# Optimization experiments

Measured on AMD Instinct MI355X. Metric: run time of the kernel, lower is better.

## Reference

```python
import jax, jax.numpy as jnp
import numpy as np
from jax import lax

WIN_SIZE = 11
SIGMA = 1.5
WEIGHTS = jnp.array([0.0448, 0.2856, 0.3001, 0.2363, 0.1333], dtype=jnp.float32)
C1 = (0.01 * 1.0) ** 2  # val_range = 1.0
C2 = (0.03 * 1.0) ** 2


def gaussian_kernel2d(kernel_size, sigma):
    g = jnp.arange(kernel_size, dtype=jnp.float32) - kernel_size // 2
    g = jnp.exp(-(g ** 2) / (2.0 * sigma ** 2))
    g = g / g.sum()
    return jnp.outer(g, g)  # [k, k]


def depthwise_conv(x, k2d):
    # x: [B, C, H, W]; same gaussian window applied per-channel (groups=C), VALID padding
    C = x.shape[1]
    w = jnp.broadcast_to(k2d, (C, 1) + k2d.shape).astype(x.dtype)
    return lax.conv_general_dilated(x, w, (1, 1), 'VALID',
                                    feature_group_count=C,
                                    dimension_numbers=('NCHW', 'OIHW', 'NCHW'))


def ssim_index(x, y, k2d, nonnegative=True):
    # returns (ss, cs) each of shape [B, C] (spatial mean, per channel)
    m1 = depthwise_conv(x, k2d)
    m2 = depthwise_conv(y, k2d)
    m12 = m1 * m2
    m1s = m1 * m1
    m2s = m2 * m2
    v1 = depthwise_conv(x * x, k2d) - m1s
    v2 = depthwise_conv(y * y, k2d) - m2s
    cov = depthwise_conv(x * y, k2d) - m12
    cs = (2.0 * cov + C2) / (v1 + v2 + C2)
    ss = (2.0 * m12 + C1) / (m1s + m2s + C1) * cs
    ss = ss.reshape(ss.shape[0], ss.shape[1], -1).mean(axis=-1)
    cs = cs.reshape(cs.shape[0], cs.shape[1], -1).mean(axis=-1)
    if nonnegative:
        ss = jnp.maximum(ss, 0.0)
        cs = jnp.maximum(cs, 0.0)
    return ss, cs


def avg_pool2(x):
    # F.avg_pool2d(kernel_size=2). Input spatial dims are even at every scale
    # (512 -> 32), so ceil_mode never pads; plain 2x2/2 mean pooling is exact.
    s = lax.reduce_window(x, jnp.array(0.0, x.dtype), lax.add,
                          (1, 1, 2, 2), (1, 1, 2, 2), 'VALID')
    return s * 0.25


def setup_inputs() -> dict:
    key = jax.random.key(0)
    k1, k2 = jax.random.split(key)
    B, C, H, W = 4, 12, 512, 512
    pred = jax.random.normal(k1, (B, C, H, W), dtype=jnp.float32)
    target = jax.random.randint(k2, (B, H, W), 0, C, dtype=jnp.int64)
    return {"pred": pred, "target": target}


def reference(pred, target):
    # MS_SSIMLoss.forward with process_input=True, nonnegative=True.
    # The per-class python loop in the original is an independent depthwise
    # computation per channel -> vectorized here as a C-channel grouped conv;
    # loss = mean over classes of (1 - mean over batch of msss) == 1 - mean(msss).
    num_classes = pred.shape[1]
    x = jax.nn.softmax(pred, axis=1)
    y = jax.nn.one_hot(target, num_classes, dtype=pred.dtype).transpose(0, 3, 1, 2)
    k2d = gaussian_kernel2d(WIN_SIZE, SIGMA)
    m = WEIGHTS.shape[0]
    vals = []
    for i in range(m):
        if i > 0:
            x = avg_pool2(x)
            y = avg_pool2(y)
        ss, cs = ssim_index(x, y, k2d, nonnegative=True)
        vals.append(cs if i + 1 < m else ss)
    stacked = jnp.stack(vals, axis=-1)  # [B, C, m]
    msss = jnp.prod(stacked ** WEIGHTS, axis=-1)  # [B, C]
    return 1.0 - msss.mean()
```

## Files before the change

### kernel.cpp

```cpp
#include <hip/hip_runtime.h>

#define NCH 12
#define NB  4
#define BC  48
#define HW0 (512 * 512)

#define GK_INIT { 0.00102840f, 0.00759863f, 0.03600078f, 0.10936081f, \
                  0.21300541f, 0.26601164f, 0.21300541f, 0.10936081f, \
                  0.03600078f, 0.00759863f, 0.00102840f }

__global__ __launch_bounds__(256)
void k_prep(const float* __restrict__ pred, const int* __restrict__ tgt,
            float* __restrict__ U, float* __restrict__ X1,
            unsigned short* __restrict__ Y1, double* __restrict__ acc) {
    if (blockIdx.x == 0) {
        for (int t = threadIdx.x; t < 480; t += 256) acc[t] = 0.0;
    }
    const int blk = blockIdx.x;
    const int b  = blk >> 8;
    const int py = blk & 255;
    const int px = threadIdx.x;
    const size_t o00 = (size_t)(2 * py) * 512 + 2 * px;
    const size_t o10 = o00 + 512;
    const float* Pb = pred + (size_t)b * NCH * HW0;

    float ex[NCH], ey[NCH], ez[NCH], ew[NCH];
    float s00 = 0.f, s01 = 0.f, s10 = 0.f, s11 = 0.f;
#pragma unroll
    for (int c = 0; c < NCH; ++c) {
        const float* pc = Pb + (size_t)c * HW0;
        float2 r0 = *(const float2*)(pc + o00);
        float2 r1 = *(const float2*)(pc + o10);
        ex[c] = __expf(r0.x); ey[c] = __expf(r0.y);
        ez[c] = __expf(r1.x); ew[c] = __expf(r1.y);
        s00 += ex[c]; s01 += ey[c]; s10 += ez[c]; s11 += ew[c];
    }
    float u00 = 1.f / s00, u01 = 1.f / s01, u10 = 1.f / s10, u11 = 1.f / s11;
    float* Ub = U + (size_t)b * HW0;
    *(float2*)(Ub + o00) = make_float2(u00, u01);
    *(float2*)(Ub + o10) = make_float2(u10, u11);

    const int* Tb = tgt + (size_t)b * HW0;
    int2 t0 = *(const int2*)(Tb + o00);
    int2 t1 = *(const int2*)(Tb + o10);

#pragma unroll
    for (int c = 0; c < NCH; ++c) {
        float xs = ex[c] * u00 + ey[c] * u01 + ez[c] * u10 + ew[c] * u11;
        size_t oidx = ((size_t)(b * NCH + c) * 256 + py) * 256 + px;
        X1[oidx] = 0.25f * xs;
        unsigned cnt = (unsigned)(t0.x == c) + (unsigned)(t0.y == c)
                     + (unsigned)(t1.x == c) + (unsigned)(t1.y == c);
        Y1[oidx] = (unsigned short)(cnt << 6);
    }
}

union SMem {
    struct {
        float sx[42 * 43 + 4];
        uint2 tm4[42 * 35];
        unsigned long long ybits[30];
        float red[8];
    } s0;
    struct {
        unsigned int sxy[42 * 43 + 4];
        uint2 tm4[42 * 35];
        unsigned short tm5[42 * 35];
        float red[8];
    } rg;
};

__device__ __forceinline__ void ssim0_tile(
    const float* __restrict__ pred, const float* __restrict__ U,
    const int* __restrict__ tgt, double* __restrict__ acc,
    int tile, int bc,
    float* sx, uint2* tm4, unsigned long long* ybits, float* red) {
    constexpr int SS = 43;
    constexpr int TS = 35;
    constexpr int H = 512, W = 512, OH = 502, OW = 502, tilesX = 16;
    const float gk[11] = GK_INIT;

    const int ty = tile / tilesX, tx = tile - ty * tilesX;
    const int oy = ty * 32, ox = tx * 32;
    const int tid = threadIdx.x;
    const bool interior = (oy + 41 < H) && (ox + 41 < W);

    const int b = bc / NCH, cls = bc - (bc / NCH) * NCH;
    const float* Pb = pred + (((size_t)b * NCH + cls) << 18);
    const float* Ub = U + ((size_t)b << 18);
    const int* Tb = tgt + ((size_t)b << 18);

    {
        int r = tid / 42, c = tid - (tid / 42) * 42;
#pragma unroll
        for (int k = 0; k < 7; ++k) {
            bool inr = (k < 6) || (tid < 228);
            int gy = oy + r, gx = ox + c;
            bool ld = inr && (interior || (gy < H && gx < W));
            float xv = 0.f;
            bool bit = false;
            if (ld) {
                int off = gy * W + gx;
                xv = __expf(Pb[off]) * Ub[off];
                bit = (Tb[off] == cls);
            }
            unsigned long long mk = __ballot(bit);
            if ((tid & 63) == 0) ybits[(tid >> 6) + (k << 2)] = mk;
            if (inr) sx[r * SS + c] = xv;
            c += 4; r += 6;
            if (c >= 42) { c -= 42; r += 1; }
        }
        if (tid == 0) { ybits[28] = 0ull; ybits[29] = 0ull; }
    }
    __syncthreads();

    if (tid < 252) {
        int rr = tid / 6, s = tid - (tid / 6) * 6;
        int c0 = s * 6;
        const float* px = sx + rr * SS + c0;
        float ac0[6] = {}, ac1[6] = {}, ac2[6] = {}, ac3[6] = {};
        unsigned long long win;
        {
            int i0 = rr * 42 + c0;
            int w = i0 >> 6, sh = i0 & 63;
            unsigned long long lo = ybits[w], hi = ybits[w + 1];
            win = sh ? ((lo >> sh) | (hi << (64 - sh))) : lo;
        }
#pragma unroll
        for (int j = 0; j < 16; ++j) {
            float xv = px[j];
            float xx = xv * xv;
            bool bit = (win >> j) & 1;
            float yv = bit ? 1.f : 0.f;
            float xy = bit ? xv : 0.f;
#pragma unroll
            for (int o = 0; o < 6; ++o) {
                int kk = j - o;
                if (kk >= 0 && kk <= 10) {
                    float g = gk[kk];
                    ac0[o] = fmaf(g, xv, ac0[o]);
                    ac1[o] = fmaf(g, yv, ac1[o]);
                    ac2[o] = fmaf(g, xx, ac2[o]);
                    ac3[o] = fmaf(g, xy, ac3[o]);
                }
            }
        }
        int ob = rr * TS + c0;
#pragma unroll
        for (int o = 0; o < 6; ++o) {
            if (c0 + o < 32) {
                unsigned ua = __float_as_uint(ac0[o]);
                unsigned ub = __float_as_uint(ac1[o]);
                unsigned uc = __float_as_uint(ac2[o]);
                unsigned ud = __float_as_uint(ac3[o]);
                tm4[ob + o] = make_uint2((ua >> 16) | (ub & 0xFFFF0000u),
                                         (uc >> 16) | (ud & 0xFFFF0000u));
            }
        }
    }
    __syncthreads();

    const float C1 = 1e-4f, C2 = 9e-4f;
    const int cc = tid & 31, rg = tid >> 5, r0 = rg << 2;
    float a0[4] = {}, a1[4] = {}, a2[4] = {}, a3[4] = {};
    const int vb = r0 * TS + cc;
#pragma unroll
    for (int k = 0; k < 14; ++k) {
        uint2 tv = tm4[vb + k * TS];
        float m1v = __uint_as_float(tv.x << 16);
        float m2v = __uint_as_float(tv.x & 0xFFFF0000u);
        float xxv = __uint_as_float(tv.y << 16);
        float xyv = __uint_as_float(tv.y & 0xFFFF0000u);
#pragma unroll
        for (int j = 0; j < 4; ++j) {
            int kk = k - j;
            if (kk >= 0 && kk <= 10) {
                float g = gk[kk];
                a0[j] = fmaf(g, m1v, a0[j]);
                a1[j] = fmaf(g, m2v, a1[j]);
                a2[j] = fmaf(g, xxv, a2[j]);
                a3[j] = fmaf(g, xyv, a3[j]);
            }
        }
    }
    float cs_l = 0.f, ss_l = 0.f;
    const bool colok = (ox + cc < OW);
#pragma unroll
    for (int j = 0; j < 4; ++j) {
        if (colok && (oy + r0 + j < OH)) {
            float m1 = a0[j], m2 = a1[j];
            float sxx = a2[j], sxy_ = a3[j];
            float m11 = m1 * m1, m22 = m2 * m2, m12 = m1 * m2;
            float v1 = sxx - m11, v2 = m2 - m22, cov = sxy_ - m12;
            float d1 = m11 + m22 + C1, d2 = v1 + v2 + C2;
            float n2 = 2.f * cov + C2;
            float q = 1.f / (d1 * d2);
            cs_l = fmaf(n2 * d1, q, cs_l);
            ss_l = fmaf((2.f * m12 + C1) * n2, q, ss_l);
        }
    }

    for (int off = 32; off; off >>= 1) {
        cs_l += __shfl_down(cs_l, off);
        ss_l += __shfl_down(ss_l, off);
    }
    int wv = tid >> 6, ln = tid & 63;
    if (ln == 0) { red[wv] = cs_l; red[4 + wv] = ss_l; }
    __syncthreads();
    if (tid == 0) {
        double cs_b = (double)red[0] + (double)red[1] + (double)red[2] + (double)red[3];
        double ss_b = (double)red[4] + (double)red[5] + (double)red[6] + (double)red[7];
        atomicAdd(&acc[bc], cs_b);
        atomicAdd(&acc[48 + bc], ss_b);
    }
}

template <int PIN>
__device__ __forceinline__ void ssim_tile_g(
    const float* __restrict__ Xs, const unsigned short* __restrict__ Ys,
    int H, int W, int OH, int OW, int tilesX, int tile, int bc,
    double* __restrict__ acc, int scale,
    unsigned int* sxy, uint2* tm4, unsigned short* tm5, float* red) {
    constexpr int SS = 43;
    constexpr int TS = 35;
    const float gk[11] = GK_INIT;

    const int ty = tile / tilesX, tx = tile - ty * tilesX;
    const int oy = ty * 32, ox = tx * 32;
    const int tid = threadIdx.x;
    const bool interior = (oy + 41 < H) && (ox + 41 < W);

    constexpr int SC = 1 << PIN;
    const int SW = W * SC;
    const float* Xb = Xs + (size_t)bc * H * W * SC * SC;
    const unsigned short* Yb = Ys + (size_t)bc * H * W * SC * SC;

    {
        int r = tid / 42, c = tid - (tid / 42) * 42;
#pragma unroll
        for (int k = 0; k < 7; ++k) {
            bool inr = (k < 6) || (tid < 228);
            int gy = oy + r, gx = ox + c;
            bool ld = inr && (interior || (gy < H && gx < W));
            float xv = 0.f;
            unsigned yc = 0;
            if (ld) {
                if constexpr (PIN == 0) {
                    int off = gy * SW + gx;
                    xv = Xb[off];
                    yc = Yb[off];
                } else {
                    const float* q = Xb + (SC * gy) * SW + SC * gx;
                    const unsigned short* qy = Yb + (SC * gy) * SW + SC * gx;
                    float s = 0.f; unsigned us = 0;
#pragma unroll
                    for (int a = 0; a < SC; ++a) {
                        const float* qr = q + a * SW;
                        const unsigned short* qyr = qy + a * SW;
                        if constexpr (PIN == 1) {
                            float2 f = *(const float2*)qr;
                            s += f.x + f.y;
                            ushort2 uy = *(const ushort2*)qyr;
                            us += (unsigned)uy.x + (unsigned)uy.y;
                        } else {
#pragma unroll
                            for (int e4 = 0; e4 < SC / 4; ++e4) {
                                float4 f = *(const float4*)(qr + e4 * 4);
                                s += (f.x + f.y) + (f.z + f.w);
                                ushort4 uy = *(const ushort4*)(qyr + e4 * 4);
                                us += ((unsigned)uy.x + (unsigned)uy.y)
                                    + ((unsigned)uy.z + (unsigned)uy.w);
                            }
                        }
                    }
                    xv = s * (1.f / (float)(SC * SC));
                    yc = us >> (2 * PIN);
                }
            }
            if (inr) {
                unsigned xb = (__float_as_uint(xv) + 0x8000u) >> 16;
                sxy[r * SS + c] = (yc << 16) | xb;
            }
            c += 4; r += 6;
            if (c >= 42) { c -= 42; r += 1; }
        }
    }
    __syncthreads();

    if (tid < 252) {
        int rr = tid / 6, s = tid - (tid / 6) * 6;
        int c0 = s * 6;
        const unsigned int* pxy = sxy + rr * SS + c0;
        float ac0[6] = {}, ac1[6] = {}, ac2[6] = {}, ac3[6] = {}, ac4[6] = {};
#pragma unroll
        for (int j = 0; j < 16; ++j) {
            unsigned v = pxy[j];
            float xv = __uint_as_float(v << 16);
            float yv = (float)(v >> 16);
            float xx = xv * xv;
            float xy = xv * yv;
            float yy = yv * yv;
#pragma unroll
            for (int o = 0; o < 6; ++o) {
                int kk = j - o;
                if (kk >= 0 && kk <= 10) {
                    float g = gk[kk];
                    ac0[o] = fmaf(g, xv, ac0[o]);
                    ac1[o] = fmaf(g, yv, ac1[o]);
                    ac2[o] = fmaf(g, xx, ac2[o]);
                    ac3[o] = fmaf(g, xy, ac3[o]);
                    ac4[o] = fmaf(g, yy, ac4[o]);
                }
            }
        }
        int ob = rr * TS + c0;
#pragma unroll
        for (int o = 0; o < 6; ++o) {
            if (c0 + o < 32) {
                unsigned ua = __float_as_uint(ac0[o]) + 0x8000u;
                unsigned ub = __float_as_uint(ac1[o]) + 0x8000u;
                unsigned uc = __float_as_uint(ac2[o]) + 0x8000u;
                unsigned ud = __float_as_uint(ac3[o]) + 0x8000u;
                unsigned ue = __float_as_uint(ac4[o]) + 0x8000u;
                tm4[ob + o] = make_uint2((ua >> 16) | (ub & 0xFFFF0000u),
                                         (uc >> 16) | (ud & 0xFFFF0000u));
                tm5[ob + o] = (unsigned short)(ue >> 16);
            }
        }
    }
    __syncthreads();

    const float C1 = 1e-4f, C2 = 9e-4f;
    const int cc = tid & 31, rg = tid >> 5, r0 = rg << 2;
    float a0[4] = {}, a1[4] = {}, a2[4] = {}, a3[4] = {}, a4[4] = {};
    const int vb = r0 * TS + cc;
#pragma unroll
    for (int k = 0; k < 14; ++k) {
        uint2 tv = tm4[vb + k * TS];
        float t0 = __uint_as_float(tv.x << 16);
        float t1 = __uint_as_float(tv.x & 0xFFFF0000u);
        float t2 = __uint_as_float(tv.y << 16);
        float t3 = __uint_as_float(tv.y & 0xFFFF0000u);
        float t4 = __uint_as_float((unsigned)tm5[vb + k * TS] << 16);
#pragma unroll
        for (int j = 0; j < 4; ++j) {
            int kk = k - j;
            if (kk >= 0 && kk <= 10) {
                float g = gk[kk];
                a0[j] = fmaf(g, t0, a0[j]);
                a1[j] = fmaf(g, t1, a1[j]);
                a2[j] = fmaf(g, t2, a2[j]);
                a3[j] = fmaf(g, t3, a3[j]);
                a4[j] = fmaf(g, t4, a4[j]);
            }
        }
    }
    float cs_l = 0.f, ss_l = 0.f;
    const bool colok = (ox + cc < OW);
#pragma unroll
    for (int j = 0; j < 4; ++j) {
        if (colok && (oy + r0 + j < OH)) {
            float m1 = a0[j];
            float m2 = a1[j] * (1.f / 256.f);
            float sxx = a2[j];
            float sxy_ = a3[j] * (1.f / 256.f);
            float syy_ = a4[j] * (1.f / 65536.f);
            float m11 = m1 * m1, m22 = m2 * m2, m12 = m1 * m2;
            float v1 = sxx - m11, v2 = syy_ - m22, cov = sxy_ - m12;
            float d1 = m11 + m22 + C1, d2 = v1 + v2 + C2;
            float n2 = 2.f * cov + C2;
            float q = 1.f / (d1 * d2);
            cs_l = fmaf(n2 * d1, q, cs_l);
            ss_l = fmaf((2.f * m12 + C1) * n2, q, ss_l);
        }
    }

    for (int offs = 32; offs; offs >>= 1) {
        cs_l += __shfl_down(cs_l, offs);
        ss_l += __shfl_down(ss_l, offs);
    }
    int wv = tid >> 6, ln = tid & 63;
    if (ln == 0) { red[wv] = cs_l; red[4 + wv] = ss_l; }
    __syncthreads();
    if (tid == 0) {
        double cs_b = (double)red[0] + (double)red[1] + (double)red[2] + (double)red[3];
        double ss_b = (double)red[4] + (double)red[5] + (double)red[6] + (double)red[7];
        atomicAdd(&acc[scale * 96 + bc], cs_b);
        atomicAdd(&acc[scale * 96 + 48 + bc], ss_b);
    }
}

__global__ __launch_bounds__(256, 7)
void k_main(const float* __restrict__ pred, const float* __restrict__ U,
            const int* __restrict__ tgt,
            const float* __restrict__ X1, const unsigned short* __restrict__ Y1,
            double* __restrict__ acc) {
    __shared__ SMem sm;
    const int gb = blockIdx.x;

    int s0_idx = -1, rest_idx = -1;
    if (gb < 16320) {
        int r = gb & 3, q = gb >> 2;
        if (r == 0) rest_idx = q;
        else        s0_idx = 3 * q + (r - 1);
    } else {
        s0_idx = 12240 + (gb - 16320);
    }

    if (s0_idx >= 0) {
        ssim0_tile(pred, U, tgt, acc, s0_idx & 255, s0_idx >> 8,
                   sm.s0.sx, sm.s0.tm4, sm.s0.ybits, sm.s0.red);
        return;
    }
    const int gq = rest_idx;
    if (gq < 48) {
        ssim_tile_g<3>(X1, Y1, 32, 32, 22, 22, 1, 0, gq,
                       acc, 4, sm.rg.sxy, sm.rg.tm4, sm.rg.tm5, sm.rg.red);
    } else if (gq < 240) {
        int t = gq - 48;
        ssim_tile_g<2>(X1, Y1, 64, 64, 54, 54, 2, t & 3, t >> 2,
                       acc, 3, sm.rg.sxy, sm.rg.tm4, sm.rg.tm5, sm.rg.red);
    } else if (gq < 1008) {
        int t = gq - 240;
        ssim_tile_g<1>(X1, Y1, 128, 128, 118, 118, 4, t & 15, t >> 4,
                       acc, 2, sm.rg.sxy, sm.rg.tm4, sm.rg.tm5, sm.rg.red);
    } else {
        int t = gq - 1008;
        ssim_tile_g<0>(X1, Y1, 256, 256, 246, 246, 8, t & 63, t >> 6,
                       acc, 1, sm.rg.sxy, sm.rg.tm4, sm.rg.tm5, sm.rg.red);
    }
}

__global__ void k_final(const double* __restrict__ acc, float* __restrict__ out) {
    const float wts[5] = {0.0448f, 0.2856f, 0.3001f, 0.2363f, 0.1333f};
    const float cnt[5] = {252004.f, 60516.f, 13924.f, 2916.f, 484.f};
    int tid = threadIdx.x;
    float msss = 0.f;
    if (tid < BC) {
        msss = 1.f;
#pragma unroll
        for (int s = 0; s < 5; ++s) {
            double a = (s < 4) ? acc[s * 96 + tid] : acc[s * 96 + 48 + tid];
            float v = fmaxf((float)(a / (double)cnt[s]), 0.f);
            msss *= powf(v, wts[s]);
        }
    }
    for (int off = 32; off; off >>= 1) msss += __shfl_down(msss, off);
    if (tid == 0) out[0] = 1.f - msss * (1.f / (float)BC);
}

extern "C" void kernel_launch(void* const* d_in, const int* in_sizes, int n_in,
                              void* d_out, int out_size, void* d_ws, size_t ws_size,
                              hipStream_t stream) {
    const float* pred = (const float*)d_in[0];
    const int*   tgt  = (const int*)d_in[1];
    float* out = (float*)d_out;

    double* acc = (double*)d_ws;
    float* U  = (float*)(acc + 480);
    float* X1 = U + (size_t)NB * HW0;
    unsigned short* Y1 = (unsigned short*)(X1 + (size_t)BC * 65536);

    k_prep<<<1024, 256, 0, stream>>>(pred, tgt, U, X1, Y1, acc);

    k_main<<<16368, 256, 0, stream>>>(pred, U, tgt, X1, Y1, acc);

    k_final<<<1, 64, 0, stream>>>(acc, out);
}
```

Measured before the change: 222.3 us.

## Drop precomputed half-res pyramid; pool scales directly from pred and target

The prep kernel now only computes the per-pixel softmax denominators. It no longer writes the half-resolution X1/Y1 arrays. Each coarser-scale tile now rebuilds its pooled softmax and one-hot inputs directly from full-resolution pred, U and target by recomputing exp and counting class matches. This removes the X1/Y1 write and re-read traffic and makes the prep kernel lighter. In exchange, the coarse tiles read far more raw data, up to 16x16 full-res pixels per pooled sample, and recompute exponentials redundantly.

```diff
diff --git a/kernel.cpp b/kernel.cpp
--- a/kernel.cpp
+++ b/kernel.cpp
@@ -9,50 +9,26 @@
                   0.21300541f, 0.26601164f, 0.21300541f, 0.10936081f, \
                   0.03600078f, 0.00759863f, 0.00102840f }
 
-__global__ __launch_bounds__(256)
-void k_prep(const float* __restrict__ pred, const int* __restrict__ tgt,
-            float* __restrict__ U, float* __restrict__ X1,
-            unsigned short* __restrict__ Y1, double* __restrict__ acc) {
+__global__ void k_denom(const float4* __restrict__ pred, float4* __restrict__ U,
+                        double* __restrict__ acc) {
     if (blockIdx.x == 0) {
         for (int t = threadIdx.x; t < 480; t += 256) acc[t] = 0.0;
     }
-    const int blk = blockIdx.x;
-    const int b  = blk >> 8;
-    const int py = blk & 255;
-    const int px = threadIdx.x;
-    const size_t o00 = (size_t)(2 * py) * 512 + 2 * px;
-    const size_t o10 = o00 + 512;
-    const float* Pb = pred + (size_t)b * NCH * HW0;
-
-    float ex[NCH], ey[NCH], ez[NCH], ew[NCH];
-    float s00 = 0.f, s01 = 0.f, s10 = 0.f, s11 = 0.f;
+    int i = blockIdx.x * blockDim.x + threadIdx.x;
+    if (i >= NB * (HW0 / 4)) return;
+    int b = i >> 16;
+    int p = i & 65535;
+    const float4* base = pred + (((size_t)b * NCH) << 16) + p;
+    float4 s = make_float4(0.f, 0.f, 0.f, 0.f);
 #pragma unroll
     for (int c = 0; c < NCH; ++c) {
-        const float* pc = Pb + (size_t)c * HW0;
-        float2 r0 = *(const float2*)(pc + o00);
-        float2 r1 = *(const float2*)(pc + o10);
-        ex[c] = __expf(r0.x); ey[c] = __expf(r0.y);
-        ez[c] = __expf(r1.x); ew[c] = __expf(r1.y);
-        s00 += ex[c]; s01 += ey[c]; s10 += ez[c]; s11 += ew[c];
-    }
-    float u00 = 1.f / s00, u01 = 1.f / s01, u10 = 1.f / s10, u11 = 1.f / s11;
-    float* Ub = U + (size_t)b * HW0;
-    *(float2*)(Ub + o00) = make_float2(u00, u01);
-    *(float2*)(Ub + o10) = make_float2(u10, u11);
-
-    const int* Tb = tgt + (size_t)b * HW0;
-    int2 t0 = *(const int2*)(Tb + o00);
-    int2 t1 = *(const int2*)(Tb + o10);
-
-#pragma unroll
-    for (int c = 0; c < NCH; ++c) {
-        float xs = ex[c] * u00 + ey[c] * u01 + ez[c] * u10 + ew[c] * u11;
-        size_t oidx = ((size_t)(b * NCH + c) * 256 + py) * 256 + px;
-        X1[oidx] = 0.25f * xs;
-        unsigned cnt = (unsigned)(t0.x == c) + (unsigned)(t0.y == c)
-                     + (unsigned)(t1.x == c) + (unsigned)(t1.y == c);
-        Y1[oidx] = (unsigned short)(cnt << 6);
-    }
+        float4 v = base[(size_t)c << 16];
+        s.x += __expf(v.x); s.y += __expf(v.y);
+        s.z += __expf(v.z); s.w += __expf(v.w);
+    }
+    float4 u;
+    u.x = 1.f / s.x; u.y = 1.f / s.y; u.z = 1.f / s.z; u.w = 1.f / s.w;
+    U[((size_t)b << 16) + p] = u;
 }
 
 union SMem {
@@ -215,25 +191,29 @@
     }
 }
 
-template <int PIN>
-__device__ __forceinline__ void ssim_tile_g(
-    const float* __restrict__ Xs, const unsigned short* __restrict__ Ys,
-    int H, int W, int OH, int OW, int tilesX, int tile, int bc,
-    double* __restrict__ acc, int scale,
+template <int S>
+__device__ __forceinline__ void ssim_rest_tile(
+    const float* __restrict__ pred, const float* __restrict__ U,
+    const int* __restrict__ tgt, double* __restrict__ acc,
+    int tile, int bc,
     unsigned int* sxy, uint2* tm4, unsigned short* tm5, float* red) {
     constexpr int SS = 43;
     constexpr int TS = 35;
+    constexpr int SC = 1 << S;
+    constexpr int H = 512 >> S;
+    constexpr int OH = H - 10;
+    constexpr int txs = (S == 1) ? 3 : (S == 2) ? 2 : (S == 3) ? 1 : 0;
     const float gk[11] = GK_INIT;
 
-    const int ty = tile / tilesX, tx = tile - ty * tilesX;
+    const int ty = tile >> txs, tx = tile & ((1 << txs) - 1);
     const int oy = ty * 32, ox = tx * 32;
     const int tid = threadIdx.x;
-    const bool interior = (oy + 41 < H) && (ox + 41 < W);
-
-    constexpr int SC = 1 << PIN;
-    const int SW = W * SC;
-    const float* Xb = Xs + (size_t)bc * H * W * SC * SC;
-    const unsigned short* Yb = Ys + (size_t)bc * H * W * SC * SC;
+    const bool interior = (oy + 41 < H) && (ox + 41 < H);
+
+    const int b = bc / NCH, cls = bc - (bc / NCH) * NCH;
+    const float* Pb = pred + (((size_t)b * NCH + cls) << 18);
+    const float* Ub = U + ((size_t)b << 18);
+    const int* Tb = tgt + ((size_t)b << 18);
 
     {
         int r = tid / 42, c = tid - (tid / 42) * 42;
@@ -241,41 +221,40 @@
         for (int k = 0; k < 7; ++k) {
             bool inr = (k < 6) || (tid < 228);
             int gy = oy + r, gx = ox + c;
-            bool ld = inr && (interior || (gy < H && gx < W));
+            bool ld = inr && (interior || (gy < H && gx < H));
             float xv = 0.f;
             unsigned yc = 0;
             if (ld) {
-                if constexpr (PIN == 0) {
-                    int off = gy * SW + gx;
-                    xv = Xb[off];
-                    yc = Yb[off];
-                } else {
-                    const float* q = Xb + (SC * gy) * SW + SC * gx;
-                    const unsigned short* qy = Yb + (SC * gy) * SW + SC * gx;
-                    float s = 0.f; unsigned us = 0;
-#pragma unroll
-                    for (int a = 0; a < SC; ++a) {
-                        const float* qr = q + a * SW;
-                        const unsigned short* qyr = qy + a * SW;
-                        if constexpr (PIN == 1) {
-                            float2 f = *(const float2*)qr;
-                            s += f.x + f.y;
-                            ushort2 uy = *(const ushort2*)qyr;
-                            us += (unsigned)uy.x + (unsigned)uy.y;
-                        } else {
-#pragma unroll
-                            for (int e4 = 0; e4 < SC / 4; ++e4) {
-                                float4 f = *(const float4*)(qr + e4 * 4);
-                                s += (f.x + f.y) + (f.z + f.w);
-                                ushort4 uy = *(const ushort4*)(qyr + e4 * 4);
-                                us += ((unsigned)uy.x + (unsigned)uy.y)
-                                    + ((unsigned)uy.z + (unsigned)uy.w);
-                            }
+                const float* qp = Pb + (size_t)(SC * gy) * 512 + SC * gx;
+                const float* qu = Ub + (size_t)(SC * gy) * 512 + SC * gx;
+                const int*   qt = Tb + (size_t)(SC * gy) * 512 + SC * gx;
+                float s = 0.f; unsigned cnt = 0;
+#pragma unroll
+                for (int a = 0; a < SC; ++a) {
+                    const float* pr = qp + a * 512;
+                    const float* ur = qu + a * 512;
+                    const int*   tr = qt + a * 512;
+                    if constexpr (SC == 2) {
+                        float2 p2 = *(const float2*)pr;
+                        float2 u2 = *(const float2*)ur;
+                        s += __expf(p2.x) * u2.x + __expf(p2.y) * u2.y;
+                        int2 t2 = *(const int2*)tr;
+                        cnt += (unsigned)(t2.x == cls) + (unsigned)(t2.y == cls);
+                    } else {
+#pragma unroll
+                        for (int e = 0; e < SC / 4; ++e) {
+                            float4 p4 = *(const float4*)(pr + 4 * e);
+                            float4 u4 = *(const float4*)(ur + 4 * e);
+                            s += __expf(p4.x) * u4.x + __expf(p4.y) * u4.y
+                               + __expf(p4.z) * u4.z + __expf(p4.w) * u4.w;
+                            int4 t4 = *(const int4*)(tr + 4 * e);
+                            cnt += ((unsigned)(t4.x == cls) + (unsigned)(t4.y == cls))
+                                 + ((unsigned)(t4.z == cls) + (unsigned)(t4.w == cls));
                         }
                     }
-                    xv = s * (1.f / (float)(SC * SC));
-                    yc = us >> (2 * PIN);
                 }
+                xv = s * (1.f / (float)(SC * SC));
+                yc = cnt << (8 - 2 * S);
             }
             if (inr) {
                 unsigned xb = (__float_as_uint(xv) + 0x8000u) >> 16;
@@ -356,7 +335,7 @@
         }
     }
     float cs_l = 0.f, ss_l = 0.f;
-    const bool colok = (ox + cc < OW);
+    const bool colok = (ox + cc < OH);
 #pragma unroll
     for (int j = 0; j < 4; ++j) {
         if (colok && (oy + r0 + j < OH)) {
@@ -385,16 +364,14 @@
     if (tid == 0) {
         double cs_b = (double)red[0] + (double)red[1] + (double)red[2] + (double)red[3];
         double ss_b = (double)red[4] + (double)red[5] + (double)red[6] + (double)red[7];
-        atomicAdd(&acc[scale * 96 + bc], cs_b);
-        atomicAdd(&acc[scale * 96 + 48 + bc], ss_b);
+        atomicAdd(&acc[S * 96 + bc], cs_b);
+        atomicAdd(&acc[S * 96 + 48 + bc], ss_b);
     }
 }
 
 __global__ __launch_bounds__(256, 7)
 void k_main(const float* __restrict__ pred, const float* __restrict__ U,
-            const int* __restrict__ tgt,
-            const float* __restrict__ X1, const unsigned short* __restrict__ Y1,
-            double* __restrict__ acc) {
+            const int* __restrict__ tgt, double* __restrict__ acc) {
     __shared__ SMem sm;
     const int gb = blockIdx.x;
 
@@ -414,20 +391,20 @@
     }
     const int gq = rest_idx;
     if (gq < 48) {
-        ssim_tile_g<3>(X1, Y1, 32, 32, 22, 22, 1, 0, gq,
-                       acc, 4, sm.rg.sxy, sm.rg.tm4, sm.rg.tm5, sm.rg.red);
+        ssim_rest_tile<4>(pred, U, tgt, acc, 0, gq,
+                          sm.rg.sxy, sm.rg.tm4, sm.rg.tm5, sm.rg.red);
     } else if (gq < 240) {
         int t = gq - 48;
-        ssim_tile_g<2>(X1, Y1, 64, 64, 54, 54, 2, t & 3, t >> 2,
-                       acc, 3, sm.rg.sxy, sm.rg.tm4, sm.rg.tm5, sm.rg.red);
+        ssim_rest_tile<3>(pred, U, tgt, acc, t & 3, t >> 2,
+                          sm.rg.sxy, sm.rg.tm4, sm.rg.tm5, sm.rg.red);
     } else if (gq < 1008) {
         int t = gq - 240;
-        ssim_tile_g<1>(X1, Y1, 128, 128, 118, 118, 4, t & 15, t >> 4,
-                       acc, 2, sm.rg.sxy, sm.rg.tm4, sm.rg.tm5, sm.rg.red);
+        ssim_rest_tile<2>(pred, U, tgt, acc, t & 15, t >> 4,
+                          sm.rg.sxy, sm.rg.tm4, sm.rg.tm5, sm.rg.red);
     } else {
         int t = gq - 1008;
-        ssim_tile_g<0>(X1, Y1, 256, 256, 246, 246, 8, t & 63, t >> 6,
-                       acc, 1, sm.rg.sxy, sm.rg.tm4, sm.rg.tm5, sm.rg.red);
+        ssim_rest_tile<1>(pred, U, tgt, acc, t & 63, t >> 6,
+                          sm.rg.sxy, sm.rg.tm4, sm.rg.tm5, sm.rg.red);
     }
 }
 
@@ -458,12 +435,11 @@
 
     double* acc = (double*)d_ws;
     float* U  = (float*)(acc + 480);
-    float* X1 = U + (size_t)NB * HW0;
-    unsigned short* Y1 = (unsigned short*)(X1 + (size_t)BC * 65536);
-
-    k_prep<<<1024, 256, 0, stream>>>(pred, tgt, U, X1, Y1, acc);
-
-    k_main<<<16368, 256, 0, stream>>>(pred, U, tgt, X1, Y1, acc);
+
+    k_denom<<<(NB * (HW0 / 4) + 255) / 256, 256, 0, stream>>>(
+        (const float4*)pred, (float4*)U, acc);
+
+    k_main<<<16368, 256, 0, stream>>>(pred, U, tgt, acc);
 
     k_final<<<1, 64, 0, stream>>>(acc, out);
 }
```

Measured after the change: 387.9 us. 74.5% more time.
